# Performance work log

Measured on AMD Instinct MI355X. Metric: run time of the kernel, lower is better.

## Reference

```python
import jax, jax.numpy as jnp
import numpy as np

# Model dims (match init_kwargs)
B, H, W, C = 16, 6, 4096, 128
OVERLAP, NUM_PVQS, NUM_RVQS = 4, 3, 6
CB_DIM, CB_SIZE = 8, 1024
FIX = H * C                          # fix_dim = in_freq*in_dim = 768
HIDDEN = FIX * OVERLAP // NUM_PVQS   # 1024 per product group


def setup_inputs() -> dict:
    key = jax.random.key(0)
    k1, k2, k3, k4 = jax.random.split(key, 4)
    return {
        "z_e": jax.random.normal(k1, (B, H * W, C), jnp.float32),
        # per-(product-group, residual-stage) codebooks
        "embeds": jax.random.normal(k2, (NUM_PVQS, NUM_RVQS, CB_SIZE, CB_DIM), jnp.float32),
        # nn.Linear(hidden, codebook_dim, bias=False) stored as (hidden, cb_dim) so y = x @ W
        "proj_down": jax.random.normal(k3, (NUM_PVQS, HIDDEN, CB_DIM), jnp.float32) * (HIDDEN ** -0.5),
        "proj_up": jax.random.normal(k4, (NUM_PVQS, CB_DIM, HIDDEN), jnp.float32) * (CB_DIM ** -0.5),
        "num_streams": 6,
    }


def _l2n(x, eps=1e-12):
    return x / jnp.maximum(jnp.linalg.norm(x, axis=-1, keepdims=True), eps)


def _codebook(residual, embed):
    """One VQ codebook (l2norm variant): cdist + argmin + lookup + ST estimator.
    residual: (B, T, d); embed: (K, d)."""
    z = _l2n(residual)
    e = _l2n(embed)
    # squared euclidean distances (B, T, K)
    d = (z * z).sum(-1, keepdims=True) - 2.0 * jnp.einsum('btd,kd->btk', z, e) + (e * e).sum(-1)
    code = jnp.argmin(d, axis=-1)                      # (B, T) int
    q = jnp.take(e, code, axis=0)                      # (B, T, d)
    cb_loss = jnp.mean((q - jax.lax.stop_gradient(residual)) ** 2)
    cm_loss = jnp.mean((residual - jax.lax.stop_gradient(q)) ** 2)
    z_q = residual + jax.lax.stop_gradient(q - residual)   # straight-through
    return z_q, code, cb_loss, cm_loss


def reference(z_e, embeds, proj_down, proj_up, num_streams):
    # pre_process (dims=3): 'b (h w) c -> b w (c h)' then fold overlap frames
    x = z_e.reshape(B, H, W, C).transpose(0, 2, 3, 1).reshape(B, W, FIX)
    T = W // OVERLAP
    x = x.reshape(B, T, OVERLAP * FIX)

    zq_parts, code_parts = [], []
    cb_loss = 0.0
    cm_loss = 0.0
    for m in range(NUM_PVQS):
        xm = x[..., m * HIDDEN:(m + 1) * HIDDEN]
        residual = xm @ proj_down[m]                   # (B, T, CB_DIM)
        zq_m = jnp.zeros_like(residual)
        codes_m = []
        for i in range(num_streams):                   # residual VQ stages
            qi, ci, cb, cm = _codebook(residual, embeds[m, i])
            residual = residual - qi
            zq_m = zq_m + qi
            codes_m.append(ci)
            cb_loss = cb_loss + cb
            cm_loss = cm_loss + cm
        zq_parts.append(zq_m @ proj_up[m])             # (B, T, HIDDEN)
        code_parts.append(jnp.stack(codes_m, axis=1))  # (B, num_streams, T)

    zq = jnp.concatenate(zq_parts, axis=-1)            # (B, T, OVERLAP*FIX)
    codes = jnp.stack(code_parts, axis=2)              # (B, num_streams, num_pvqs, T)

    # post_process (dims=3): unfold overlap, 'b w (c h) -> b (h w) c'
    zq = zq.reshape(B, W, FIX).reshape(B, W, C, H).transpose(0, 3, 1, 2).reshape(B, H * W, C)
    return zq, codes, cb_loss / NUM_PVQS, cm_loss / NUM_PVQS
```

## Files before the change

### kernel.cpp

```cpp
#include <hip/hip_runtime.h>

#define BB        16
#define HH        6
#define WW        4096
#define CC        128
#define TT        1024
#define NTOK      16384
#define FIX       768
#define HID       1024
#define CBK       1024
#define CBD       8
#define NPVQ      3
#define NRVQ      6
#define ZQ_SIZE   50331648ull

#define OFF_ACC   0ull
#define OFF_EN64  16ull
#define OFF_EN32  (OFF_EN64 + 1179648ull)
#define OFF_PUT   (OFF_EN32 + 589824ull)
#define OFF_R     (OFF_PUT + 98304ull)
#define OFF_ZQ    (OFF_R + 3145728ull)

typedef float v2f __attribute__((ext_vector_type(2)));

__device__ __forceinline__ float dot32(const float* __restrict__ row,
                                       const v2f rn2[4]) {
    const float4* p4 = (const float4*)row;
    float4 e0 = p4[0], e1 = p4[1];
    v2f acc = {0.0f, 0.0f};
    v2f p;
    p.x = e0.x; p.y = e0.y; acc = __builtin_elementwise_fma(rn2[0], p, acc);
    p.x = e0.z; p.y = e0.w; acc = __builtin_elementwise_fma(rn2[1], p, acc);
    p.x = e1.x; p.y = e1.y; acc = __builtin_elementwise_fma(rn2[2], p, acc);
    p.x = e1.z; p.y = e1.w; acc = __builtin_elementwise_fma(rn2[3], p, acc);
    return acc.x + acc.y;
}

__global__ __launch_bounds__(256) void knorm(const float* __restrict__ emb,
                                             double* __restrict__ en64,
                                             float* __restrict__ en32) {
    int gid = blockIdx.x * 256 + threadIdx.x;
    if (gid >= NPVQ * NRVQ * CBK) return;
    const float* e = emb + (size_t)gid * CBD;
    double v[CBD];
    double s = 0.0;
#pragma unroll
    for (int d = 0; d < CBD; ++d) { v[d] = (double)e[d]; s += v[d] * v[d]; }
    double n = fmax(sqrt(s), 1e-12);
#pragma unroll
    for (int d = 0; d < CBD; ++d) {
        double q = v[d] / n;
        en64[(size_t)gid * CBD + d] = q;
        en32[(size_t)gid * CBD + d] = (float)q;
    }
}

__global__ __launch_bounds__(256) void kputr(const float* __restrict__ pu,
                                             float* __restrict__ pu_t) {
    int gid = blockIdx.x * 256 + threadIdx.x;
    if (gid >= NPVQ * CBD * HID) return;
    int j = gid & (HID - 1), md = gid >> 10;
    int m = md >> 3, d = md & 7;
    pu_t[((size_t)m * HID + j) * CBD + d] = pu[gid];
}

__global__ __launch_bounds__(384) void kproj(const float* __restrict__ ze,
                                             const float* __restrict__ pd,
                                             double* __restrict__ r_ws) {
    __shared__ float x[2][NPVQ * HID];
    const int tok0 = blockIdx.x * 2;
    const int b = tok0 >> 10, t0 = tok0 & 1023;
    const int tid = threadIdx.x;
    const size_t zbase = (size_t)b * (HH * WW * CC);
#pragma unroll
    for (int q = 0; q < 4; ++q) {
        int g = tid + 384 * q;
        int tk = g >= 768;
        int gg = g - tk * 768;
        int h = gg >> 7, v = gg & 127;
        const float4 val = *(const float4*)(ze + zbase + (size_t)(h * WW + (t0 + tk) * 4) * CC + v * 4);
        float vv[4] = {val.x, val.y, val.z, val.w};
#pragma unroll
        for (int e = 0; e < 4; ++e) {
            int oc = v * 4 + e, o = oc >> 7, c = oc & 127;
            x[tk][o * FIX + c * HH + h] = vv[e];
        }
    }
    __syncthreads();
    const int w = tid >> 6, l = tid & 63;
    const int tk = w >= 3, m = w - tk * 3;
    double acc[CBD] = {0, 0, 0, 0, 0, 0, 0, 0};
    for (int q = 0; q < 16; ++q) {
        int j = l + 64 * q;
        double xv = (double)x[tk][m * HID + j];
        const float* pr = pd + (size_t)(m * HID + j) * CBD;
#pragma unroll
        for (int d = 0; d < CBD; ++d) acc[d] = fma(xv, (double)pr[d], acc[d]);
    }
#pragma unroll
    for (int off = 32; off >= 1; off >>= 1) {
#pragma unroll
        for (int d = 0; d < CBD; ++d) acc[d] += __shfl_down(acc[d], off, 64);
    }
    if (l == 0) {
        double* rp = r_ws + ((size_t)m * NTOK + tok0 + tk) * CBD;
#pragma unroll
        for (int d = 0; d < CBD; ++d) rp[d] = acc[d];
    }
}

#define KV_WAVES    8
#define KV_THREADS  (KV_WAVES * 64)
#define KV_WSLICE   (CBK / KV_WAVES)
#define KV_EPS      2e-6f
#define KV_EPS_CAND 2e-6f

__global__ __launch_bounds__(KV_THREADS) void kvq(const double* __restrict__ en_all,
                                                  const float* __restrict__ es_all,
                                                  const double* __restrict__ r_ws,
                                                  float* __restrict__ zq_ws,
                                                  float* __restrict__ out,
                                                  const int* __restrict__ nsp,
                                                  double* __restrict__ accum) {
    __shared__ __align__(16) float tbl[CBK * CBD];
    __shared__ float  mb1[KV_THREADS];
    __shared__ float  mb2[KV_THREADS];
    __shared__ int    mbk[KV_THREADS];
    __shared__ double md64[KV_THREADS];
    __shared__ int    mk64[KV_THREADS];

    const int blk = blockIdx.x;
    const int m = blk >> 8, g = blk & 255;
    const int tid = threadIdx.x;
    const int w = tid >> 6, l = tid & 63;
    const int tok = g * 64 + l;
    const int b = tok >> 10, t = tok & 1023;
    const int ns = *nsp;

    double r[CBD];
    {
        const double* rp = r_ws + ((size_t)m * NTOK + tok) * CBD;
#pragma unroll
        for (int d = 0; d < CBD; ++d) r[d] = rp[d];
    }
    double zq[CBD] = {0, 0, 0, 0, 0, 0, 0, 0};
    double loss = 0.0;

    const int kl0 = w * KV_WSLICE;
    for (int i = 0; i < ns; ++i) {
        const double* en = en_all + ((size_t)(m * NRVQ + i)) * CBK * CBD;
        const float*  es = es_all + ((size_t)(m * NRVQ + i)) * CBK * CBD;
        double s = 0.0;
#pragma unroll
        for (int d = 0; d < CBD; ++d) s += r[d] * r[d];
        double inv = 1.0 / fmax(sqrt(s), 1e-12);
        v2f rn2[4];
#pragma unroll
        for (int d = 0; d < CBD; d += 2) {
            rn2[d >> 1].x = (float)(r[d] * inv);
            rn2[d >> 1].y = (float)(r[d + 1] * inv);
        }

        __syncthreads();
        {
            const float4* src = (const float4*)es;
            float4* dst = (float4*)tbl;
#pragma unroll
            for (int q = 0; q < 4; ++q) dst[tid + KV_THREADS * q] = src[tid + KV_THREADS * q];
        }
        __syncthreads();

        float b1 = -1e30f, b2 = -1e30f;
        int bk = kl0;
        for (int k = kl0; k < kl0 + KV_WSLICE; k += 4) {
            float dots[4];
#pragma unroll
            for (int u = 0; u < 4; ++u)
                dots[u] = dot32(tbl + (size_t)(k + u) * CBD, rn2);
#pragma unroll
            for (int u = 0; u < 4; ++u) {
                float dv = dots[u];
                if (dv > b1) { b2 = b1; b1 = dv; bk = k + u; }
                else if (dv > b2) { b2 = dv; }
            }
        }
        mb1[tid] = b1; mb2[tid] = b2; mbk[tid] = bk;
        __syncthreads();
        float B1 = mb1[l], B2 = mb2[l];
        int K = mbk[l];
#pragma unroll
        for (int w2 = 1; w2 < KV_WAVES; ++w2) {
            float c1 = mb1[w2 * 64 + l];
            float c2 = mb2[w2 * 64 + l];
            int   ck = mbk[w2 * 64 + l];
            if (c1 > B1) { B2 = fmaxf(B1, c2); B1 = c1; K = ck; }
            else         { B2 = fmaxf(B2, c1); }
        }
        int bbk = K;
        bool uncert = (B1 - B2) <= KV_EPS;
        if (__any(uncert)) {
            __syncthreads();
            double rb = -1e300;
            int rk = CBK;
            for (int k = kl0; k < kl0 + KV_WSLICE; ++k) {
                float dv = dot32(tbl + (size_t)k * CBD, rn2);
                if (uncert && dv >= B1 - KV_EPS_CAND) {
                    const double* e64 = en + (size_t)k * CBD;
                    double q0 = 0.0, q1 = 0.0;
#pragma unroll
                    for (int d = 0; d < CBD; d += 2) {
                        q0 = fma(r[d], e64[d], q0);
                        q1 = fma(r[d + 1], e64[d + 1], q1);
                    }
                    double dot = q0 + q1;
                    if (dot > rb || (dot == rb && k < rk)) { rb = dot; rk = k; }
                }
            }
            md64[tid] = rb; mk64[tid] = rk;
            __syncthreads();
            if (uncert) {
                double R = md64[l];
                int RK = mk64[l];
#pragma unroll
                for (int w2 = 1; w2 < KV_WAVES; ++w2) {
                    double d2 = md64[w2 * 64 + l];
                    int    k2 = mk64[w2 * 64 + l];
                    if (d2 > R || (d2 == R && k2 < RK)) { R = d2; RK = k2; }
                }
                bbk = RK;
            }
        }
        const double* qv = en + (size_t)bbk * CBD;
        if (w == 0) {
            double ls = 0.0;
#pragma unroll
            for (int d = 0; d < CBD; ++d) { double df = qv[d] - r[d]; ls += df * df; }
            loss += ls;
            out[ZQ_SIZE + ((size_t)(b * ns + i) * NPVQ + m) * TT + t] = (float)bbk;
        }
#pragma unroll
        for (int d = 0; d < CBD; ++d) { double q = qv[d]; r[d] -= q; zq[d] += q; }
    }

    if (w == 0) {
        float* zp = zq_ws + ((size_t)m * NTOK + tok) * CBD;
#pragma unroll
        for (int d = 0; d < CBD; ++d) zp[d] = (float)zq[d];
#pragma unroll
        for (int off = 32; off >= 1; off >>= 1) loss += __shfl_down(loss, off, 64);
        if (l == 0) atomicAdd(accum, loss);
    }
}

__global__ __launch_bounds__(256) void kout(const float* __restrict__ pu_t,
                                            const float* __restrict__ zq_ws,
                                            float* __restrict__ out,
                                            const int* __restrict__ nsp,
                                            const double* __restrict__ accum) {
    __shared__ float zl[32][NPVQ][CBD];
    const int blk = blockIdx.x;
    const int tok0 = blk * 32;
    const int b = tok0 >> 10, t0 = tok0 & 1023;
    const int tid = threadIdx.x;
#pragma unroll
    for (int q = 0; q < 3; ++q) {
        int ii = tid + 256 * q;
        int mm = ii >> 8, rem = ii & 255, tt = rem >> 3, d = rem & 7;
        zl[tt][mm][d] = zq_ws[((size_t)mm * NTOK + tok0 + tt) * CBD + d];
    }
    __syncthreads();
    const size_t obase = (size_t)b * (HH * WW * CC);
#pragma unroll 2
    for (int q = 0; q < 12; ++q) {
        int idx = tid + 256 * q;
        int h = idx >> 9, rem = idx & 511, o = rem >> 7, c = rem & 127;
        int f = o * FIX + c * HH + h;
        int m = f >> 10, j = f & 1023;
        const float4* p4 = (const float4*)(pu_t + ((size_t)m * HID + j) * CBD);
        float4 pa = p4[0], pb = p4[1];
        float pu8[CBD] = {pa.x, pa.y, pa.z, pa.w, pb.x, pb.y, pb.z, pb.w};
        size_t rowbase = obase + ((size_t)h * WW + t0 * 4 + o) * CC + c;
        for (int tt = 0; tt < 32; ++tt) {
            float y = 0.0f;
#pragma unroll
            for (int d = 0; d < CBD; ++d) y = fmaf(zl[tt][m][d], pu8[d], y);
            out[rowbase + (size_t)tt * 4 * CC] = y;
        }
    }
    if (blk == 0 && tid == 0) {
        int ns = *nsp;
        double s = *accum;
        float lv = (float)(s / (double)(NTOK * CBD * NPVQ));
        size_t lbase = ZQ_SIZE + (size_t)BB * ns * NPVQ * TT;
        out[lbase] = lv;
        out[lbase + 1] = lv;
    }
}

extern "C" void kernel_launch(void* const* d_in, const int* in_sizes, int n_in,
                              void* d_out, int out_size, void* d_ws, size_t ws_size,
                              hipStream_t stream) {
    const float* ze  = (const float*)d_in[0];
    const float* emb = (const float*)d_in[1];
    const float* pd  = (const float*)d_in[2];
    const float* pu  = (const float*)d_in[3];
    const int*   nsp = (const int*)d_in[4];
    float* out = (float*)d_out;
    char* ws = (char*)d_ws;

    double* accum = (double*)(ws + OFF_ACC);
    double* en64  = (double*)(ws + OFF_EN64);
    float*  en32  = (float*)(ws + OFF_EN32);
    float*  pu_t  = (float*)(ws + OFF_PUT);
    double* r_ws  = (double*)(ws + OFF_R);
    float*  zq_ws = (float*)(ws + OFF_ZQ);

    hipMemsetAsync(accum, 0, 16, stream);
    knorm<<<(NPVQ * NRVQ * CBK + 255) / 256, 256, 0, stream>>>(emb, en64, en32);
    kputr<<<(NPVQ * CBD * HID + 255) / 256, 256, 0, stream>>>(pu, pu_t);
    kproj<<<NTOK / 2, 384, 0, stream>>>(ze, pd, r_ws);
    kvq<<<NPVQ * (NTOK / 64), KV_THREADS, 0, stream>>>(en64, en32, r_ws, zq_ws, out, nsp, accum);
    kout<<<NTOK / 32, 256, 0, stream>>>(pu_t, zq_ws, out, nsp, accum);
}
```

Measured before the change: 330.0 us.

## Fuse down-projection into VQ kernel with precomputed gather offsets

Removes the separate projection kernel and its double-precision residual workspace round trip. Each VQ block now computes its 64 tokens' down-projections itself, using scalar gathers from z_e through a precomputed offset table, and stages the results in LDS. It also adds an occupancy hint to the VQ kernel, keeps the zq accumulator in float, and vectorizes the codebook dot and the output up-projection with packed float2 FMAs. The gathers read z_e with strided, uncoalesced scalar loads instead of the previous float4 loads, which may cost more memory traffic than the removed round trip saves.

```diff
diff --git a/kernel.cpp b/kernel.cpp
--- a/kernel.cpp
+++ b/kernel.cpp
@@ -18,15 +18,13 @@
 #define OFF_EN64  16ull
 #define OFF_EN32  (OFF_EN64 + 1179648ull)
 #define OFF_PUT   (OFF_EN32 + 589824ull)
-#define OFF_R     (OFF_PUT + 98304ull)
-#define OFF_ZQ    (OFF_R + 3145728ull)
+#define OFF_OFF0  (OFF_PUT + 98304ull)
+#define OFF_ZQ    (OFF_OFF0 + 12288ull)
 
 typedef float v2f __attribute__((ext_vector_type(2)));
 
-__device__ __forceinline__ float dot32(const float* __restrict__ row,
-                                       const v2f rn2[4]) {
-    const float4* p4 = (const float4*)row;
-    float4 e0 = p4[0], e1 = p4[1];
+__device__ __forceinline__ float dot32v(const float4 e0, const float4 e1,
+                                        const v2f rn2[4]) {
     v2f acc = {0.0f, 0.0f};
     v2f p;
     p.x = e0.x; p.y = e0.y; acc = __builtin_elementwise_fma(rn2[0], p, acc);
@@ -64,49 +62,12 @@
     pu_t[((size_t)m * HID + j) * CBD + d] = pu[gid];
 }
 
-__global__ __launch_bounds__(384) void kproj(const float* __restrict__ ze,
-                                             const float* __restrict__ pd,
-                                             double* __restrict__ r_ws) {
-    __shared__ float x[2][NPVQ * HID];
-    const int tok0 = blockIdx.x * 2;
-    const int b = tok0 >> 10, t0 = tok0 & 1023;
-    const int tid = threadIdx.x;
-    const size_t zbase = (size_t)b * (HH * WW * CC);
-#pragma unroll
-    for (int q = 0; q < 4; ++q) {
-        int g = tid + 384 * q;
-        int tk = g >= 768;
-        int gg = g - tk * 768;
-        int h = gg >> 7, v = gg & 127;
-        const float4 val = *(const float4*)(ze + zbase + (size_t)(h * WW + (t0 + tk) * 4) * CC + v * 4);
-        float vv[4] = {val.x, val.y, val.z, val.w};
-#pragma unroll
-        for (int e = 0; e < 4; ++e) {
-            int oc = v * 4 + e, o = oc >> 7, c = oc & 127;
-            x[tk][o * FIX + c * HH + h] = vv[e];
-        }
-    }
-    __syncthreads();
-    const int w = tid >> 6, l = tid & 63;
-    const int tk = w >= 3, m = w - tk * 3;
-    double acc[CBD] = {0, 0, 0, 0, 0, 0, 0, 0};
-    for (int q = 0; q < 16; ++q) {
-        int j = l + 64 * q;
-        double xv = (double)x[tk][m * HID + j];
-        const float* pr = pd + (size_t)(m * HID + j) * CBD;
-#pragma unroll
-        for (int d = 0; d < CBD; ++d) acc[d] = fma(xv, (double)pr[d], acc[d]);
-    }
-#pragma unroll
-    for (int off = 32; off >= 1; off >>= 1) {
-#pragma unroll
-        for (int d = 0; d < CBD; ++d) acc[d] += __shfl_down(acc[d], off, 64);
-    }
-    if (l == 0) {
-        double* rp = r_ws + ((size_t)m * NTOK + tok0 + tk) * CBD;
-#pragma unroll
-        for (int d = 0; d < CBD; ++d) rp[d] = acc[d];
-    }
+__global__ __launch_bounds__(256) void koff(int* __restrict__ off0) {
+    int p = blockIdx.x * 256 + threadIdx.x;
+    if (p >= NPVQ * HID) return;
+    int o = p / FIX, rem = p - o * FIX;
+    int c = rem / HH, h = rem - c * HH;
+    off0[p] = h * (WW * CC) + o * CC + c;
 }
 
 #define KV_WAVES    8
@@ -115,19 +76,22 @@
 #define KV_EPS      2e-6f
 #define KV_EPS_CAND 2e-6f
 
-__global__ __launch_bounds__(KV_THREADS) void kvq(const double* __restrict__ en_all,
-                                                  const float* __restrict__ es_all,
-                                                  const double* __restrict__ r_ws,
-                                                  float* __restrict__ zq_ws,
-                                                  float* __restrict__ out,
-                                                  const int* __restrict__ nsp,
-                                                  double* __restrict__ accum) {
+__global__ __launch_bounds__(KV_THREADS, 2) void kvq(const double* __restrict__ en_all,
+                                                     const float* __restrict__ es_all,
+                                                     const float* __restrict__ ze,
+                                                     const float* __restrict__ pd,
+                                                     const int* __restrict__ off0g,
+                                                     float* __restrict__ zq_ws,
+                                                     float* __restrict__ out,
+                                                     const int* __restrict__ nsp,
+                                                     double* __restrict__ accum) {
     __shared__ __align__(16) float tbl[CBK * CBD];
     __shared__ float  mb1[KV_THREADS];
     __shared__ float  mb2[KV_THREADS];
     __shared__ int    mbk[KV_THREADS];
     __shared__ double md64[KV_THREADS];
     __shared__ int    mk64[KV_THREADS];
+    __shared__ __align__(16) double r_lds[64][CBD];
 
     const int blk = blockIdx.x;
     const int m = blk >> 8, g = blk & 255;
@@ -137,13 +101,52 @@
     const int b = tok >> 10, t = tok & 1023;
     const int ns = *nsp;
 
+    {
+        const size_t zb = (size_t)((g * 64) >> 10) * (HH * WW * CC);
+#pragma unroll
+        for (int pair = 0; pair < 4; ++pair) {
+            const int tokA = g * 64 + w * 8 + pair * 2;
+            const int tA = tokA & 1023, tB = (tokA + 1) & 1023;
+            double acc0[CBD] = {0, 0, 0, 0, 0, 0, 0, 0};
+            double acc1[CBD] = {0, 0, 0, 0, 0, 0, 0, 0};
+            for (int q = 0; q < 16; ++q) {
+                int j = l + 64 * q;
+                int off = off0g[m * HID + j];
+                float xa = ze[zb + (size_t)tA * 512 + off];
+                float xb = ze[zb + (size_t)tB * 512 + off];
+                const float* pr = pd + ((size_t)m * HID + j) * CBD;
+#pragma unroll
+                for (int d = 0; d < CBD; ++d) {
+                    double pv = (double)pr[d];
+                    acc0[d] = fma((double)xa, pv, acc0[d]);
+                    acc1[d] = fma((double)xb, pv, acc1[d]);
+                }
+            }
+#pragma unroll
+            for (int off = 32; off >= 1; off >>= 1) {
+#pragma unroll
+                for (int d = 0; d < CBD; ++d) {
+                    acc0[d] += __shfl_down(acc0[d], off, 64);
+                    acc1[d] += __shfl_down(acc1[d], off, 64);
+                }
+            }
+            if (l == 0) {
+#pragma unroll
+                for (int d = 0; d < CBD; ++d) {
+                    r_lds[w * 8 + pair * 2][d]     = acc0[d];
+                    r_lds[w * 8 + pair * 2 + 1][d] = acc1[d];
+                }
+            }
+        }
+    }
+    __syncthreads();
     double r[CBD];
-    {
-        const double* rp = r_ws + ((size_t)m * NTOK + tok) * CBD;
-#pragma unroll
-        for (int d = 0; d < CBD; ++d) r[d] = rp[d];
-    }
-    double zq[CBD] = {0, 0, 0, 0, 0, 0, 0, 0};
+#pragma unroll
+    for (int d = 0; d < CBD; ++d) r[d] = r_lds[l][d];
+
+    float zq[CBD];
+#pragma unroll
+    for (int d = 0; d < CBD; ++d) zq[d] = 0.0f;
     double loss = 0.0;
 
     const int kl0 = w * KV_WSLICE;
@@ -173,10 +176,12 @@
         float b1 = -1e30f, b2 = -1e30f;
         int bk = kl0;
         for (int k = kl0; k < kl0 + KV_WSLICE; k += 4) {
+            const float4* pA = (const float4*)(tbl + (size_t)k * CBD);
             float dots[4];
-#pragma unroll
-            for (int u = 0; u < 4; ++u)
-                dots[u] = dot32(tbl + (size_t)(k + u) * CBD, rn2);
+            dots[0] = dot32v(pA[0], pA[1], rn2);
+            dots[1] = dot32v(pA[2], pA[3], rn2);
+            dots[2] = dot32v(pA[4], pA[5], rn2);
+            dots[3] = dot32v(pA[6], pA[7], rn2);
 #pragma unroll
             for (int u = 0; u < 4; ++u) {
                 float dv = dots[u];
@@ -203,7 +208,8 @@
             double rb = -1e300;
             int rk = CBK;
             for (int k = kl0; k < kl0 + KV_WSLICE; ++k) {
-                float dv = dot32(tbl + (size_t)k * CBD, rn2);
+                const float4* pA = (const float4*)(tbl + (size_t)k * CBD);
+                float dv = dot32v(pA[0], pA[1], rn2);
                 if (uncert && dv >= B1 - KV_EPS_CAND) {
                     const double* e64 = en + (size_t)k * CBD;
                     double q0 = 0.0, q1 = 0.0;
@@ -239,13 +245,17 @@
             out[ZQ_SIZE + ((size_t)(b * ns + i) * NPVQ + m) * TT + t] = (float)bbk;
         }
 #pragma unroll
-        for (int d = 0; d < CBD; ++d) { double q = qv[d]; r[d] -= q; zq[d] += q; }
+        for (int d = 0; d < CBD; ++d) {
+            double q = qv[d];
+            r[d] -= q;
+            zq[d] += (float)q;
+        }
     }
 
     if (w == 0) {
         float* zp = zq_ws + ((size_t)m * NTOK + tok) * CBD;
 #pragma unroll
-        for (int d = 0; d < CBD; ++d) zp[d] = (float)zq[d];
+        for (int d = 0; d < CBD; ++d) zp[d] = zq[d];
 #pragma unroll
         for (int off = 32; off >= 1; off >>= 1) loss += __shfl_down(loss, off, 64);
         if (l == 0) atomicAdd(accum, loss);
@@ -278,13 +288,22 @@
         int m = f >> 10, j = f & 1023;
         const float4* p4 = (const float4*)(pu_t + ((size_t)m * HID + j) * CBD);
         float4 pa = p4[0], pb = p4[1];
-        float pu8[CBD] = {pa.x, pa.y, pa.z, pa.w, pb.x, pb.y, pb.z, pb.w};
+        v2f pw[4];
+        pw[0].x = pa.x; pw[0].y = pa.y;
+        pw[1].x = pa.z; pw[1].y = pa.w;
+        pw[2].x = pb.x; pw[2].y = pb.y;
+        pw[3].x = pb.z; pw[3].y = pb.w;
         size_t rowbase = obase + ((size_t)h * WW + t0 * 4 + o) * CC + c;
         for (int tt = 0; tt < 32; ++tt) {
-            float y = 0.0f;
-#pragma unroll
-            for (int d = 0; d < CBD; ++d) y = fmaf(zl[tt][m][d], pu8[d], y);
-            out[rowbase + (size_t)tt * 4 * CC] = y;
+            const float4* z4 = (const float4*)&zl[tt][m][0];
+            float4 za = z4[0], zb = z4[1];
+            v2f acc = {0.0f, 0.0f};
+            v2f zz;
+            zz.x = za.x; zz.y = za.y; acc = __builtin_elementwise_fma(zz, pw[0], acc);
+            zz.x = za.z; zz.y = za.w; acc = __builtin_elementwise_fma(zz, pw[1], acc);
+            zz.x = zb.x; zz.y = zb.y; acc = __builtin_elementwise_fma(zz, pw[2], acc);
+            zz.x = zb.z; zz.y = zb.w; acc = __builtin_elementwise_fma(zz, pw[3], acc);
+            out[rowbase + (size_t)tt * 4 * CC] = acc.x + acc.y;
         }
     }
     if (blk == 0 && tid == 0) {
@@ -312,13 +331,14 @@
     double* en64  = (double*)(ws + OFF_EN64);
     float*  en32  = (float*)(ws + OFF_EN32);
     float*  pu_t  = (float*)(ws + OFF_PUT);
-    double* r_ws  = (double*)(ws + OFF_R);
+    int*    off0g = (int*)(ws + OFF_OFF0);
     float*  zq_ws = (float*)(ws + OFF_ZQ);
 
     hipMemsetAsync(accum, 0, 16, stream);
     knorm<<<(NPVQ * NRVQ * CBK + 255) / 256, 256, 0, stream>>>(emb, en64, en32);
     kputr<<<(NPVQ * CBD * HID + 255) / 256, 256, 0, stream>>>(pu, pu_t);
-    kproj<<<NTOK / 2, 384, 0, stream>>>(ze, pd, r_ws);
-    kvq<<<NPVQ * (NTOK / 64), KV_THREADS, 0, stream>>>(en64, en32, r_ws, zq_ws, out, nsp, accum);
+    koff<<<(NPVQ * HID + 255) / 256, 256, 0, stream>>>(off0g);
+    kvq<<<NPVQ * (NTOK / 64), KV_THREADS, 0, stream>>>(en64, en32, ze, pd, off0g,
+                                                       zq_ws, out, nsp, accum);
     kout<<<NTOK / 32, 256, 0, stream>>>(pu_t, zq_ws, out, nsp, accum);
 }
```

Result: slower. 338.6 us (+2.6%).
